# Optimization experiments

Measured on AMD Instinct MI355X. Metric: run time of the kernel, lower is better.

Reference implementation:

```python
import jax, jax.numpy as jnp
import numpy as np

EPS = 1e-5
RATIO = 8


def _conv3d(x, w, b, groups=1, pad=0):
    # x: [N,C,T,H,W], w: [O, C//groups, kT,kH,kW]
    y = jax.lax.conv_general_dilated(
        x, w, window_strides=(1, 1, 1), padding=[(pad, pad)] * 3,
        dimension_numbers=("NCDHW", "OIDHW", "NCDHW"), feature_group_count=groups)
    return y + b[None, :, None, None, None]


def _dwblock(x, pw1_w, pw1_b, dw_w, dw_b, pw2_w, pw2_b):
    # pointwise1 (1x1x1) -> depthwise 3x3x3 -> pointwise2 (1x1x1)
    mid = pw1_w.shape[0]
    x = _conv3d(x, pw1_w, pw1_b)
    x = _conv3d(x, dw_w, dw_b, groups=mid, pad=1)
    x = _conv3d(x, pw2_w, pw2_b)
    return x


def _make_dw_params(key, c_in, c_out, prefix):
    mid = c_in // RATIO
    ks = jax.random.split(key, 3)
    s = 0.02
    return {
        f"{prefix}_pw1_w": jax.random.normal(ks[0], (mid, c_in, 1, 1, 1), jnp.float32) * s,
        f"{prefix}_pw1_b": jnp.zeros((mid,), jnp.float32),
        f"{prefix}_dw_w": jax.random.normal(ks[1], (mid, 1, 3, 3, 3), jnp.float32) * s,
        f"{prefix}_dw_b": jnp.zeros((mid,), jnp.float32),
        f"{prefix}_pw2_w": jax.random.normal(ks[2], (c_out, mid, 1, 1, 1), jnp.float32) * s,
        f"{prefix}_pw2_b": jnp.zeros((c_out,), jnp.float32),
    }


def setup_inputs() -> dict:
    key = jax.random.key(0)
    N, C, T, H, W = 4, 256, 16, 28, 28
    KC, VC = 128, 256
    k0, k1, k2, k3, k4 = jax.random.split(key, 5)
    inp = {"input_": jax.random.normal(k0, (N, C, T, H, W), jnp.float32)}
    inp.update(_make_dw_params(k1, C, KC, "k"))
    inp.update(_make_dw_params(k2, C, KC, "q"))
    inp.update(_make_dw_params(k3, C, VC, "v"))
    inp.update(_make_dw_params(k4, VC, C, "r"))
    return inp


HEAD_COUNT = 8


def reference(input_,
              k_pw1_w, k_pw1_b, k_dw_w, k_dw_b, k_pw2_w, k_pw2_b,
              q_pw1_w, q_pw1_b, q_dw_w, q_dw_b, q_pw2_w, q_pw2_b,
              v_pw1_w, v_pw1_b, v_dw_w, v_dw_b, v_pw2_w, v_pw2_b,
              r_pw1_w, r_pw1_b, r_dw_w, r_dw_b, r_pw2_w, r_pw2_b):
    n, c, t, h, w = input_.shape
    L = t * h * w
    Hc = HEAD_COUNT

    keys = _dwblock(input_, k_pw1_w, k_pw1_b, k_dw_w, k_dw_b, k_pw2_w, k_pw2_b)
    queries = _dwblock(input_, q_pw1_w, q_pw1_b, q_dw_w, q_dw_b, q_pw2_w, q_pw2_b)
    values = _dwblock(input_, v_pw1_w, v_pw1_b, v_dw_w, v_dw_b, v_pw2_w, v_pw2_b)

    kc = keys.shape[1]
    vc = values.shape[1]
    hk, hv = kc // Hc, vc // Hc

    # [n, heads, head_dim, L]
    K = keys.reshape(n, Hc, hk, L)
    Q = queries.reshape(n, Hc, hk, L)
    V = values.reshape(n, Hc, hv, L)

    K = jax.nn.softmax(K, axis=3)          # softmax over sequence (dim=2 in torch slice)
    Q = jax.nn.softmax(Q, axis=2)          # softmax over per-head key channels (dim=1)

    # context = K @ V^T : [n, heads, hk, hv]
    context = jnp.einsum("nhkl,nhvl->nhkv", K, V)
    # attended = context^T @ Q : [n, heads, hv, L]
    attended = jnp.einsum("nhkv,nhkl->nhvl", context, Q)
    aggregated = attended.reshape(n, vc, t, h, w)

    reproj = _dwblock(aggregated, r_pw1_w, r_pw1_b, r_dw_w, r_dw_b, r_pw2_w, r_pw2_b)
    x = reproj + input_
    # f.layer_norm(x, x.size()): normalize over the WHOLE tensor, no affine
    mu = jnp.mean(x)
    var = jnp.mean((x - mu) ** 2)
    return (x - mu) / jnp.sqrt(var + EPS)
```

## Files before the change

### kernel.cpp

```cpp
#include <hip/hip_runtime.h>
#include <cstddef>

#define NB   4
#define CIN  256
#define TT   16
#define HH   28
#define WW   28
#define LL   12544
#define MIDC 32
#define KCC  128
#define VCC  256
#define HC   8
#define HK   16
#define HV   32
#define CTXSPLIT 14
#define CTXSTR 544
#define EPSV 1e-5f
#define XPAD 264

typedef __attribute__((ext_vector_type(8))) short bf16x8;
typedef __attribute__((ext_vector_type(8))) unsigned short u16x8;
typedef __attribute__((ext_vector_type(4))) float f32x4;
typedef __attribute__((ext_vector_type(4))) unsigned short u16x4;

__device__ __forceinline__ float b2f(unsigned short u) {
    return __builtin_bit_cast(float, ((unsigned int)u) << 16);
}
__device__ __forceinline__ unsigned short f2b(float f) {
    unsigned int u = __builtin_bit_cast(unsigned int, f);
    u += 0x7FFFu + ((u >> 16) & 1u);
    return (unsigned short)(u >> 16);
}

#define XTF_N_STRIDE 3211264ull
#define MID_SET_STRIDE 1605632ull

struct WconvA { const float* w1[4]; const float* w2[4]; };
struct Pw1M  { const short* wt[3]; const float* b[3]; unsigned short* out[3]; };
struct DwA   { const unsigned short* in[3]; const float* w[3]; const float* b[3]; unsigned short* out[3]; };
struct Pw2M  { const short* w2f; const unsigned short* d; const float* b[3]; unsigned short* out[3]; };

__global__ __launch_bounds__(256) void wconv_kernel(WconvA a, short* __restrict__ w1f,
                                                    short* __restrict__ w2f)
{
    const int g = blockIdx.x*256 + threadIdx.x;
    if (g < 4096) {
        const int L = g & 63, kap = (g >> 6) & 7, mt = (g >> 9) & 1, set = g >> 10;
        const int m = 16*mt + (L & 15);
        const int c0 = 32*kap + 8*(L >> 4);
        const float* wp = a.w1[set] + m*CIN + c0;
#pragma unroll
        for (int j = 0; j < 8; ++j) w1f[(size_t)g*8 + j] = (short)f2b(wp[j]);
    } else if (g < 4096 + 3072) {
        const int g2 = g - 4096;
        const int L = g2 & 63, mtg = g2 >> 6;
        int set, mtl;
        if (mtg < 8)       { set = 0; mtl = mtg; }
        else if (mtg < 16) { set = 1; mtl = mtg - 8; }
        else if (mtg < 32) { set = 2; mtl = mtg - 16; }
        else               { set = 3; mtl = mtg - 32; }
        const int m = 16*mtl + (L & 15);
        const int c0 = 8*(L >> 4);
        const float* wp = a.w2[set] + m*MIDC + c0;
#pragma unroll
        for (int j = 0; j < 8; ++j) w2f[(size_t)g2*8 + j] = (short)f2b(wp[j]);
    }
}

__global__ __launch_bounds__(128) void pw1_lds(const float* __restrict__ in, Pw1M a)
{
    __shared__ unsigned short xs[64*XPAD];
    const int n = blockIdx.y;
    const int l0 = blockIdx.x*64;
    const int t = threadIdx.x, wid = t >> 6, lane = t & 63;
    const float* ib = in + (size_t)n*CIN*LL;

    const int lt = (t & 15)*4;
    const int cp = (t >> 4)*2;
#pragma unroll 4
    for (int cc = 0; cc < 16; ++cc) {
        const int c = cc*16 + cp;
        float4 va = *reinterpret_cast<const float4*>(ib + (size_t)c*LL + l0 + lt);
        float4 vb = *reinterpret_cast<const float4*>(ib + (size_t)(c+1)*LL + l0 + lt);
        unsigned int p0 = (unsigned int)f2b(va.x) | ((unsigned int)f2b(vb.x) << 16);
        unsigned int p1 = (unsigned int)f2b(va.y) | ((unsigned int)f2b(vb.y) << 16);
        unsigned int p2 = (unsigned int)f2b(va.z) | ((unsigned int)f2b(vb.z) << 16);
        unsigned int p3 = (unsigned int)f2b(va.w) | ((unsigned int)f2b(vb.w) << 16);
        *reinterpret_cast<unsigned int*>(&xs[(lt+0)*XPAD + c]) = p0;
        *reinterpret_cast<unsigned int*>(&xs[(lt+1)*XPAD + c]) = p1;
        *reinterpret_cast<unsigned int*>(&xs[(lt+2)*XPAD + c]) = p2;
        *reinterpret_cast<unsigned int*>(&xs[(lt+3)*XPAD + c]) = p3;
    }
    __syncthreads();

    const int colb = lane & 15, qq = lane >> 4;
    f32x4 acc[3][2][2];
#pragma unroll
    for (int s = 0; s < 3; ++s)
#pragma unroll
        for (int mt = 0; mt < 2; ++mt)
#pragma unroll
            for (int ti = 0; ti < 2; ++ti)
#pragma unroll
                for (int r = 0; r < 4; ++r) acc[s][mt][ti][r] = 0.f;

    for (int kap = 0; kap < 8; ++kap) {
        bf16x8 bfr[2];
#pragma unroll
        for (int ti = 0; ti < 2; ++ti) {
            const int ll = (wid*2 + ti)*16 + colb;
            bfr[ti] = *reinterpret_cast<const bf16x8*>(&xs[ll*XPAD + kap*32 + 8*qq]);
        }
#pragma unroll
        for (int s = 0; s < 3; ++s) {
#pragma unroll
            for (int mt = 0; mt < 2; ++mt) {
                bf16x8 afr = *reinterpret_cast<const bf16x8*>(
                    a.wt[s] + ((mt*8 + kap)*512 + lane*8));
#pragma unroll
                for (int ti = 0; ti < 2; ++ti)
                    acc[s][mt][ti] = __builtin_amdgcn_mfma_f32_16x16x32_bf16(
                        afr, bfr[ti], acc[s][mt][ti], 0, 0, 0);
            }
        }
    }
#pragma unroll
    for (int s = 0; s < 3; ++s) {
        const float* bb = a.b[s];
        unsigned short* op = a.out[s] + (size_t)n*MIDC*LL;
#pragma unroll
        for (int mt = 0; mt < 2; ++mt) {
            const int m0 = mt*16 + qq*4;
#pragma unroll
            for (int ti = 0; ti < 2; ++ti) {
                const int lg = l0 + (wid*2 + ti)*16 + colb;
#pragma unroll
                for (int r = 0; r < 4; ++r)
                    op[(size_t)(m0 + r)*LL + lg] = f2b(acc[s][mt][ti][r] + bb[m0 + r]);
            }
        }
    }
}

__global__ __launch_bounds__(256) void pw1_frag(const short* __restrict__ xtf, Pw1M a)
{
    const int n = blockIdx.y, bx = blockIdx.x;
    const int t = threadIdx.x, wid = t >> 6, lane = t & 63;
    const int mt = wid & 1, lh = wid >> 1;
    const int tau0 = bx*8 + lh*4;
    const short* xb = xtf + (size_t)n*XTF_N_STRIDE;

    f32x4 acc[4];
#pragma unroll
    for (int i = 0; i < 4; ++i)
#pragma unroll
        for (int r = 0; r < 4; ++r) acc[i][r] = 0.f;

    for (int kap = 0; kap < 8; ++kap) {
        bf16x8 afr = *reinterpret_cast<const bf16x8*>(a.wt[0] + ((mt*8 + kap)*512 + lane*8));
#pragma unroll
        for (int i = 0; i < 4; ++i) {
            bf16x8 bfr = *reinterpret_cast<const bf16x8*>(
                xb + ((size_t)((tau0 + i)*8 + kap)*512 + lane*8));
            acc[i] = __builtin_amdgcn_mfma_f32_16x16x32_bf16(afr, bfr, acc[i], 0, 0, 0);
        }
    }
    const float* bb = a.b[0];
    unsigned short* op = a.out[0] + (size_t)n*MIDC*LL;
    const int col = lane & 15;
    const int m0 = mt*16 + (lane >> 4)*4;
#pragma unroll
    for (int r = 0; r < 4; ++r) {
        const float bv = bb[m0 + r];
#pragma unroll
        for (int i = 0; i < 4; ++i)
            op[(size_t)(m0 + r)*LL + (tau0 + i)*16 + col] = f2b(acc[i][r] + bv);
    }
}

struct Row6 { float v[6]; };

__device__ __forceinline__ Row6 load_row(const unsigned short* base, int zz, int yy, int x0)
{
    Row6 r;
    const bool ok = (zz >= 0) && (zz < TT) && (yy >= 0) && (yy < HH);
    if (ok) {
        const unsigned short* p = base + zz*(HH*WW) + yy*WW + x0;
        u16x4 m4 = *reinterpret_cast<const u16x4*>(p);
        r.v[0] = (x0 > 0)  ? b2f(p[-1]) : 0.f;
        r.v[1] = b2f(m4[0]); r.v[2] = b2f(m4[1]);
        r.v[3] = b2f(m4[2]); r.v[4] = b2f(m4[3]);
        r.v[5] = (x0 < 24) ? b2f(p[4]) : 0.f;
    } else {
#pragma unroll
        for (int i = 0; i < 6; ++i) r.v[i] = 0.f;
    }
    return r;
}

__device__ __forceinline__ void acc9(float& a0, float& a1, float& a2, float& a3,
                                     const Row6* rows, const float* w9)
{
#pragma unroll
    for (int dy = 0; dy < 3; ++dy)
#pragma unroll
        for (int dx = 0; dx < 3; ++dx) {
            const float wv = w9[dy*3 + dx];
            a0 = fmaf(wv, rows[dy].v[0 + dx], a0);
            a1 = fmaf(wv, rows[dy].v[1 + dx], a1);
            a2 = fmaf(wv, rows[dy].v[2 + dx], a2);
            a3 = fmaf(wv, rows[dy].v[3 + dx], a3);
        }
}

__global__ __launch_bounds__(256) void dw_reg(DwA a)
{
    const int tid = threadIdx.x;
    if (tid >= 196) return;
    const int z  = blockIdx.z;
    const int nm = blockIdx.y;
    const int m  = nm & (MIDC-1);
    const int t0 = blockIdx.x * 8;

    const float* wp = a.w[z] + m*27;
    float wv[27];
#pragma unroll
    for (int i = 0; i < 27; ++i) wv[i] = wp[i];
    const float bias = a.b[z][m];

    const int xg = tid % 7, y = tid / 7;
    const int x0 = xg*4;
    const unsigned short* ip = a.in[z] + (size_t)nm*LL;
    unsigned short* op = a.out[z] + (size_t)nm*LL;

    Row6 win[3][3];
#pragma unroll
    for (int dy = 0; dy < 3; ++dy) {
        win[0][dy] = load_row(ip, t0-1, y+dy-1, x0);
        win[1][dy] = load_row(ip, t0,   y+dy-1, x0);
    }
#pragma unroll
    for (int tt = 0; tt < 8; ++tt) {
        const int p0 = tt % 3, p1 = (tt+1) % 3, p2 = (tt+2) % 3;
        const int znew = t0 + tt + 1;
        win[p2][0] = load_row(ip, znew, y-1, x0);
        win[p2][1] = load_row(ip, znew, y,   x0);
        win[p2][2] = load_row(ip, znew, y+1, x0);

        float a0 = bias, a1 = bias, a2 = bias, a3 = bias;
        acc9(a0, a1, a2, a3, win[p0], wv);
        acc9(a0, a1, a2, a3, win[p1], wv + 9);
        acc9(a0, a1, a2, a3, win[p2], wv + 18);

        u16x4 o4 = { f2b(a0), f2b(a1), f2b(a2), f2b(a3) };
        *reinterpret_cast<u16x4*>(op + (size_t)(t0+tt)*(HH*WW) + y*WW + x0) = o4;
    }
}

__global__ __launch_bounds__(256) void pw2_g(Pw2M a)
{
    const int z = blockIdx.z, n = blockIdx.y, bx = blockIdx.x;
    int set, chunk;
    if (z < 2)      { set = 0; chunk = z; }
    else if (z < 4) { set = 1; chunk = z - 2; }
    else            { set = 2; chunk = z - 4; }
    const int OC   = (set == 2) ? 256 : 128;
    const int off2 = (set == 0) ? 0 : (set == 1) ? 8 : 16;

    const int t = threadIdx.x, wid = t >> 6, lane = t & 63;
    const int mtile = chunk*4 + wid;
    bf16x8 afr = *reinterpret_cast<const bf16x8*>(
        a.w2f + ((size_t)(off2 + mtile)*512 + lane*8));
    const unsigned short* db = a.d + (size_t)set*MID_SET_STRIDE + (size_t)n*MIDC*LL;
    const int colb = lane & 15, c0 = 8*(lane >> 4);

    f32x4 acc[4];
#pragma unroll
    for (int i = 0; i < 4; ++i) {
#pragma unroll
        for (int r = 0; r < 4; ++r) acc[i][r] = 0.f;
        const unsigned short* p = db + (size_t)c0*LL + (bx*4 + i)*16 + colb;
        bf16x8 bfr;
#pragma unroll
        for (int j = 0; j < 8; ++j) bfr[j] = (short)p[(size_t)j*LL];
        acc[i] = __builtin_amdgcn_mfma_f32_16x16x32_bf16(afr, bfr, acc[i], 0, 0, 0);
    }
    const float* bb = a.b[set];
    unsigned short* op = a.out[set] + (size_t)n*OC*LL;
    const int m0 = 16*mtile + (lane >> 4)*4;
#pragma unroll
    for (int r = 0; r < 4; ++r) {
        const float bv = bb[m0 + r];
#pragma unroll
        for (int i = 0; i < 4; ++i)
            op[(size_t)(m0 + r)*LL + (bx*4 + i)*16 + colb] = f2b(acc[i][r] + bv);
    }
}

__global__ __launch_bounds__(256) void ctx_mfma(
    const unsigned short* __restrict__ Kb, const unsigned short* __restrict__ Vb,
    float* __restrict__ ctxp)
{
    const int nh = blockIdx.y;
    const int sp = blockIdx.x;
    const int n = nh >> 3, h = nh & 7;
    const int t = threadIdx.x, w = t >> 6, lane = t & 63;
    const int i = lane & 15, q = lane >> 4;

    const unsigned short* Kp = Kb + ((size_t)(n*KCC + h*HK))*LL;
    const unsigned short* Vp = Vb + ((size_t)(n*VCC + h*HV))*LL;

    f32x4 a0 = {0.f,0.f,0.f,0.f}, a1 = {0.f,0.f,0.f,0.f};
    float asum = 0.f;

    const int cbase = sp*28 + w*7;
#pragma unroll 2
    for (int cc = 0; cc < 7; ++cc) {
        const int l0 = (cbase + cc)*32 + 8*q;
        bf16x8 kf = *reinterpret_cast<const bf16x8*>(Kp + (size_t)i*LL + l0);
        bf16x8 pf;
#pragma unroll
        for (int j = 0; j < 8; ++j) {
            const float e = __expf(b2f((unsigned short)kf[j]));
            asum += e;
            pf[j] = (short)f2b(e);
        }
        bf16x8 b0 = *reinterpret_cast<const bf16x8*>(Vp + (size_t)i*LL + l0);
        bf16x8 b1 = *reinterpret_cast<const bf16x8*>(Vp + (size_t)(i+16)*LL + l0);
        a0 = __builtin_amdgcn_mfma_f32_16x16x32_bf16(pf, b0, a0, 0, 0, 0);
        a1 = __builtin_amdgcn_mfma_f32_16x16x32_bf16(pf, b1, a1, 0, 0, 0);
    }
    asum += __shfl_xor(asum, 16);
    asum += __shfl_xor(asum, 32);

    __shared__ float cs[4][512];
    __shared__ float as[4][16];
#pragma unroll
    for (int r = 0; r < 4; ++r) {
        cs[w][(q*4 + r)*32 + i]      = a0[r];
        cs[w][(q*4 + r)*32 + 16 + i] = a1[r];
    }
    if (q == 0) as[w][i] = asum;
    __syncthreads();
    float* cp = ctxp + ((size_t)nh*CTXSPLIT + sp)*CTXSTR;
    for (int p = t; p < 512; p += 256)
        cp[p] = cs[0][p] + cs[1][p] + cs[2][p] + cs[3][p];
    if (t < 16) cp[512 + t] = as[0][t] + as[1][t] + as[2][t] + as[3][t];
}

__global__ void ctx_reduce(const float* __restrict__ ctxp, float* __restrict__ ctx)
{
    const int idx = blockIdx.x*256 + threadIdx.x;
    const int nh = idx >> 9;
    const int p  = idx & 511;
    const int k  = p >> 5;
    float s = 0.f, se = 0.f;
    for (int sp = 0; sp < CTXSPLIT; ++sp) {
        const float* cp = ctxp + ((size_t)nh*CTXSPLIT + sp)*CTXSTR;
        s  += cp[p];
        se += cp[512 + k];
    }
    ctx[idx] = s / se;
}

__global__ __launch_bounds__(256) void attended_kernel(
    const float* __restrict__ ctx, const unsigned short* __restrict__ Qb,
    short* __restrict__ aggf)
{
    const int nh = blockIdx.y;
    const int n = nh >> 3, h = nh & 7;
    const int l = blockIdx.x*256 + threadIdx.x;
    const float* __restrict__ cl = ctx + (size_t)nh*512;

    const unsigned short* Qp = Qb + ((size_t)(n*KCC + h*HK))*LL + l;
    float q[HK];
    float mx = -1e30f;
#pragma unroll
    for (int k = 0; k < HK; ++k) { q[k] = b2f(Qp[(size_t)k*LL]); mx = fmaxf(mx, q[k]); }
    float s = 0.f;
#pragma unroll
    for (int k = 0; k < HK; ++k) { q[k] = __expf(q[k] - mx); s += q[k]; }
    const float inv = 1.f / s;
#pragma unroll
    for (int k = 0; k < HK; ++k) q[k] *= inv;

    float av[HV];
#pragma unroll 4
    for (int v = 0; v < HV; ++v) {
        float acc = 0.f;
#pragma unroll
        for (int k = 0; k < HK; ++k) acc += q[k] * cl[k*HV + v];
        av[v] = acc;
    }
    short* ob = aggf + (size_t)n*XTF_N_STRIDE + ((size_t)((l >> 4)*8 + h))*512;
#pragma unroll
    for (int qd = 0; qd < 4; ++qd) {
        bf16x8 vv;
#pragma unroll
        for (int j = 0; j < 8; ++j) vv[j] = (short)f2b(av[qd*8 + j]);
        *reinterpret_cast<bf16x8*>(ob + (qd*16 + (l & 15))*8) = vv;
    }
}

__global__ __launch_bounds__(256) void pw2r_g(
    const unsigned short* __restrict__ d, const short* __restrict__ w2f,
    const float* __restrict__ bias, const float* __restrict__ resid,
    unsigned short* __restrict__ xout, float* __restrict__ part)
{
    const int z = blockIdx.z, n = blockIdx.y, bx = blockIdx.x;
    const int t = threadIdx.x, wid = t >> 6, lane = t & 63;
    const int mtile = z*4 + wid;
    bf16x8 afr = *reinterpret_cast<const bf16x8*>(
        w2f + ((size_t)(32 + mtile)*512 + lane*8));
    const unsigned short* db = d + (size_t)n*MIDC*LL;
    const int colb = lane & 15, c0 = 8*(lane >> 4);

    f32x4 acc[4];
#pragma unroll
    for (int i = 0; i < 4; ++i) {
#pragma unroll
        for (int r = 0; r < 4; ++r) acc[i][r] = 0.f;
        const unsigned short* p = db + (size_t)c0*LL + (bx*4 + i)*16 + colb;
        bf16x8 bfr;
#pragma unroll
        for (int j = 0; j < 8; ++j) bfr[j] = (short)p[(size_t)j*LL];
        acc[i] = __builtin_amdgcn_mfma_f32_16x16x32_bf16(afr, bfr, acc[i], 0, 0, 0);
    }
    const int m0 = 16*mtile + (lane >> 4)*4;
    float s1 = 0.f, s2 = 0.f;
#pragma unroll
    for (int r = 0; r < 4; ++r) {
        const float bv = bias[m0 + r];
#pragma unroll
        for (int i = 0; i < 4; ++i) {
            const size_t off = (size_t)(n*CIN + m0 + r)*LL + (bx*4 + i)*16 + colb;
            const float v = acc[i][r] + bv + resid[off];
            xout[off] = f2b(v);
            s1 += v; s2 += v*v;
        }
    }
    __shared__ float red[256];
    const int bid = (z*NB + n)*196 + bx;
    red[t] = s1; __syncthreads();
    for (int s = 128; s > 0; s >>= 1) { if (t < s) red[t] += red[t+s]; __syncthreads(); }
    if (t == 0) part[2*bid] = red[0];
    __syncthreads();
    red[t] = s2; __syncthreads();
    for (int s = 128; s > 0; s >>= 1) { if (t < s) red[t] += red[t+s]; __syncthreads(); }
    if (t == 0) part[2*bid + 1] = red[0];
}

__global__ void stats_kernel(const float* __restrict__ part, int nblocks,
                             float* __restrict__ stats)
{
    __shared__ float r1[256], r2[256];
    const int t = threadIdx.x;
    float s1 = 0.f, s2 = 0.f;
    for (int i = t; i < nblocks; i += 256) { s1 += part[2*i]; s2 += part[2*i+1]; }
    r1[t] = s1; r2[t] = s2; __syncthreads();
    for (int s = 128; s > 0; s >>= 1) { if (t < s) { r1[t] += r1[t+s]; r2[t] += r2[t+s]; } __syncthreads(); }
    if (t == 0) {
        const float M = (float)NB*CIN*LL;
        const float mu = r1[0]/M;
        const float var = r2[0]/M - mu*mu;
        stats[0] = mu;
        stats[1] = 1.0f/sqrtf(var + EPSV);
    }
}

__global__ __launch_bounds__(256) void norm_bf16(
    const unsigned short* __restrict__ x, const float* __restrict__ stats,
    float* __restrict__ out)
{
    const float mu = stats[0], inv = stats[1];
    const size_t total = (size_t)NB*CIN*LL;
    for (size_t i = ((size_t)blockIdx.x*256 + threadIdx.x)*8; i < total;
         i += (size_t)gridDim.x*256*8) {
        u16x8 v = *reinterpret_cast<const u16x8*>(x + i);
        float4 o0, o1;
        o0.x = (b2f(v[0])-mu)*inv; o0.y = (b2f(v[1])-mu)*inv;
        o0.z = (b2f(v[2])-mu)*inv; o0.w = (b2f(v[3])-mu)*inv;
        o1.x = (b2f(v[4])-mu)*inv; o1.y = (b2f(v[5])-mu)*inv;
        o1.z = (b2f(v[6])-mu)*inv; o1.w = (b2f(v[7])-mu)*inv;
        *reinterpret_cast<float4*>(out + i)     = o0;
        *reinterpret_cast<float4*>(out + i + 4) = o1;
    }
}

extern "C" void kernel_launch(void* const* d_in, const int* in_sizes, int n_in,
                              void* d_out, int out_size, void* d_ws, size_t ws_size,
                              hipStream_t stream) {
    const float* input   = (const float*)d_in[0];
    const float* k_pw1_w = (const float*)d_in[1];
    const float* k_pw1_b = (const float*)d_in[2];
    const float* k_dw_w  = (const float*)d_in[3];
    const float* k_dw_b  = (const float*)d_in[4];
    const float* k_pw2_w = (const float*)d_in[5];
    const float* k_pw2_b = (const float*)d_in[6];
    const float* q_pw1_w = (const float*)d_in[7];
    const float* q_pw1_b = (const float*)d_in[8];
    const float* q_dw_w  = (const float*)d_in[9];
    const float* q_dw_b  = (const float*)d_in[10];
    const float* q_pw2_w = (const float*)d_in[11];
    const float* q_pw2_b = (const float*)d_in[12];
    const float* v_pw1_w = (const float*)d_in[13];
    const float* v_pw1_b = (const float*)d_in[14];
    const float* v_dw_w  = (const float*)d_in[15];
    const float* v_dw_b  = (const float*)d_in[16];
    const float* v_pw2_w = (const float*)d_in[17];
    const float* v_pw2_b = (const float*)d_in[18];
    const float* r_pw1_w = (const float*)d_in[19];
    const float* r_pw1_b = (const float*)d_in[20];
    const float* r_dw_w  = (const float*)d_in[21];
    const float* r_dw_b  = (const float*)d_in[22];
    const float* r_pw2_w = (const float*)d_in[23];
    const float* r_pw2_b = (const float*)d_in[24];

    char* base = (char*)d_ws;
    unsigned short* dbuf = (unsigned short*)base;
    short* aggf = (short*)base;
    unsigned short* midb  = (unsigned short*)(base + 25690112);
    unsigned short* mid_r = midb;
    unsigned short* d_r   = (unsigned short*)(base + 25690112 + 6422528);
    unsigned short* Kb = (unsigned short*)(base + 54591488);
    unsigned short* Qb = (unsigned short*)(base + 67436544);
    unsigned short* Vb = (unsigned short*)(base + 80281600);
    unsigned short* xb = (unsigned short*)(base + 54591488);
    char* H = base + 105971712;
    float* ctxp   = (float*)H;
    float* ctx    = (float*)(H + 974848);
    float* part   = (float*)(H + 1040384);
    float* statsp = (float*)(H + 1065472);
    short* w1f    = (short*)(H + 1065536);
    short* w2f    = (short*)(H + 1131072);

    {
        WconvA a;
        a.w1[0]=k_pw1_w; a.w1[1]=q_pw1_w; a.w1[2]=v_pw1_w; a.w1[3]=r_pw1_w;
        a.w2[0]=k_pw2_w; a.w2[1]=q_pw2_w; a.w2[2]=v_pw2_w; a.w2[3]=r_pw2_w;
        wconv_kernel<<<28, 256, 0, stream>>>(a, w1f, w2f);
    }
    {
        Pw1M a;
        a.wt[0]=w1f;        a.wt[1]=w1f+8192;   a.wt[2]=w1f+16384;
        a.b[0]=k_pw1_b;     a.b[1]=q_pw1_b;     a.b[2]=v_pw1_b;
        a.out[0]=midb;      a.out[1]=midb+MID_SET_STRIDE; a.out[2]=midb+2*MID_SET_STRIDE;
        pw1_lds<<<dim3(196, NB), 128, 0, stream>>>(input, a);
    }
    {
        DwA a;
        a.in[0]=midb; a.in[1]=midb+MID_SET_STRIDE; a.in[2]=midb+2*MID_SET_STRIDE;
        a.w[0]=k_dw_w; a.w[1]=q_dw_w; a.w[2]=v_dw_w;
        a.b[0]=k_dw_b; a.b[1]=q_dw_b; a.b[2]=v_dw_b;
        a.out[0]=dbuf; a.out[1]=dbuf+MID_SET_STRIDE; a.out[2]=dbuf+2*MID_SET_STRIDE;
        dw_reg<<<dim3(2, NB*MIDC, 3), 256, 0, stream>>>(a);
    }
    {
        Pw2M a;
        a.w2f = w2f; a.d = dbuf;
        a.b[0]=k_pw2_b; a.b[1]=q_pw2_b; a.b[2]=v_pw2_b;
        a.out[0]=Kb; a.out[1]=Qb; a.out[2]=Vb;
        pw2_g<<<dim3(196, NB, 8), 256, 0, stream>>>(a);
    }
    ctx_mfma<<<dim3(CTXSPLIT, NB*HC), 256, 0, stream>>>(Kb, Vb, ctxp);
    ctx_reduce<<<64, 256, 0, stream>>>(ctxp, ctx);
    attended_kernel<<<dim3(49, NB*HC), 256, 0, stream>>>(ctx, Qb, aggf);
    {
        Pw1M a;
        a.wt[0]=w1f+24576; a.wt[1]=a.wt[0]; a.wt[2]=a.wt[0];
        a.b[0]=r_pw1_b;    a.b[1]=a.b[0];   a.b[2]=a.b[0];
        a.out[0]=mid_r;    a.out[1]=a.out[0]; a.out[2]=a.out[0];
        pw1_frag<<<dim3(98, NB), 256, 0, stream>>>(aggf, a);
    }
    {
        DwA a;
        a.in[0]=mid_r; a.w[0]=r_dw_w; a.b[0]=r_dw_b; a.out[0]=d_r;
        a.in[1]=a.in[0]; a.w[1]=a.w[0]; a.b[1]=a.b[0]; a.out[1]=a.out[0];
        a.in[2]=a.in[0]; a.w[2]=a.w[0]; a.b[2]=a.b[0]; a.out[2]=a.out[0];
        dw_reg<<<dim3(2, NB*MIDC, 1), 256, 0, stream>>>(a);
    }
    pw2r_g<<<dim3(196, NB, 4), 256, 0, stream>>>(d_r, w2f, r_pw2_b, input, xb, part);
    stats_kernel<<<1, 256, 0, stream>>>(part, 3136, statsp);
    norm_bf16<<<2048, 256, 0, stream>>>(xb, statsp, (float*)d_out);
}
```

Baseline: 143.5 us.

## Fuse attention apply with reproj pw1 and replace reduce kernels with atomics

The context partial sums are now accumulated with atomicAdd into a buffer zeroed inside wconv_kernel, which removes ctx_reduce. The attended computation is fused with the reprojection pointwise1 MFMA through an LDS tile, so the bf16 aggregated tensor no longer round-trips through global memory. The global layer-norm statistics are reduced by atomics into 8 slots that norm_bf16 reads directly, which removes stats_kernel. Together this cuts three launches and one large intermediate buffer. The cost is that float atomics make the sums order-nondeterministic, and the large LDS tile may lower occupancy of the fused kernel.

```diff
diff --git a/kernel.cpp b/kernel.cpp
--- a/kernel.cpp
+++ b/kernel.cpp
@@ -14,9 +14,9 @@
 #define HK   16
 #define HV   32
 #define CTXSPLIT 14
-#define CTXSTR 544
 #define EPSV 1e-5f
 #define XPAD 264
+#define APAD 264
 
 typedef __attribute__((ext_vector_type(8))) short bf16x8;
 typedef __attribute__((ext_vector_type(8))) unsigned short u16x8;
@@ -32,7 +32,6 @@
     return (unsigned short)(u >> 16);
 }
 
-#define XTF_N_STRIDE 3211264ull
 #define MID_SET_STRIDE 1605632ull
 
 struct WconvA { const float* w1[4]; const float* w2[4]; };
@@ -41,9 +40,11 @@
 struct Pw2M  { const short* w2f; const unsigned short* d; const float* b[3]; unsigned short* out[3]; };
 
 __global__ __launch_bounds__(256) void wconv_kernel(WconvA a, short* __restrict__ w1f,
-                                                    short* __restrict__ w2f)
+                                                    short* __restrict__ w2f,
+                                                    float* __restrict__ zbuf)
 {
     const int g = blockIdx.x*256 + threadIdx.x;
+    for (int i = g; i < 16912; i += 28*256) zbuf[i] = 0.f;
     if (g < 4096) {
         const int L = g & 63, kap = (g >> 6) & 7, mt = (g >> 9) & 1, set = g >> 10;
         const int m = 16*mt + (L & 15);
@@ -142,42 +143,6 @@
     }
 }
 
-__global__ __launch_bounds__(256) void pw1_frag(const short* __restrict__ xtf, Pw1M a)
-{
-    const int n = blockIdx.y, bx = blockIdx.x;
-    const int t = threadIdx.x, wid = t >> 6, lane = t & 63;
-    const int mt = wid & 1, lh = wid >> 1;
-    const int tau0 = bx*8 + lh*4;
-    const short* xb = xtf + (size_t)n*XTF_N_STRIDE;
-
-    f32x4 acc[4];
-#pragma unroll
-    for (int i = 0; i < 4; ++i)
-#pragma unroll
-        for (int r = 0; r < 4; ++r) acc[i][r] = 0.f;
-
-    for (int kap = 0; kap < 8; ++kap) {
-        bf16x8 afr = *reinterpret_cast<const bf16x8*>(a.wt[0] + ((mt*8 + kap)*512 + lane*8));
-#pragma unroll
-        for (int i = 0; i < 4; ++i) {
-            bf16x8 bfr = *reinterpret_cast<const bf16x8*>(
-                xb + ((size_t)((tau0 + i)*8 + kap)*512 + lane*8));
-            acc[i] = __builtin_amdgcn_mfma_f32_16x16x32_bf16(afr, bfr, acc[i], 0, 0, 0);
-        }
-    }
-    const float* bb = a.b[0];
-    unsigned short* op = a.out[0] + (size_t)n*MIDC*LL;
-    const int col = lane & 15;
-    const int m0 = mt*16 + (lane >> 4)*4;
-#pragma unroll
-    for (int r = 0; r < 4; ++r) {
-        const float bv = bb[m0 + r];
-#pragma unroll
-        for (int i = 0; i < 4; ++i)
-            op[(size_t)(m0 + r)*LL + (tau0 + i)*16 + col] = f2b(acc[i][r] + bv);
-    }
-}
-
 struct Row6 { float v[6]; };
 
 __device__ __forceinline__ Row6 load_row(const unsigned short* base, int zz, int yy, int x0)
@@ -299,7 +264,7 @@
 
 __global__ __launch_bounds__(256) void ctx_mfma(
     const unsigned short* __restrict__ Kb, const unsigned short* __restrict__ Vb,
-    float* __restrict__ ctxp)
+    float* __restrict__ csum, float* __restrict__ sesum)
 {
     const int nh = blockIdx.y;
     const int sp = blockIdx.x;
@@ -342,70 +307,107 @@
     }
     if (q == 0) as[w][i] = asum;
     __syncthreads();
-    float* cp = ctxp + ((size_t)nh*CTXSPLIT + sp)*CTXSTR;
+    float* cp = csum + (size_t)nh*512;
     for (int p = t; p < 512; p += 256)
-        cp[p] = cs[0][p] + cs[1][p] + cs[2][p] + cs[3][p];
-    if (t < 16) cp[512 + t] = as[0][t] + as[1][t] + as[2][t] + as[3][t];
-}
-
-__global__ void ctx_reduce(const float* __restrict__ ctxp, float* __restrict__ ctx)
-{
-    const int idx = blockIdx.x*256 + threadIdx.x;
-    const int nh = idx >> 9;
-    const int p  = idx & 511;
-    const int k  = p >> 5;
-    float s = 0.f, se = 0.f;
-    for (int sp = 0; sp < CTXSPLIT; ++sp) {
-        const float* cp = ctxp + ((size_t)nh*CTXSPLIT + sp)*CTXSTR;
-        s  += cp[p];
-        se += cp[512 + k];
-    }
-    ctx[idx] = s / se;
-}
-
-__global__ __launch_bounds__(256) void attended_kernel(
-    const float* __restrict__ ctx, const unsigned short* __restrict__ Qb,
-    short* __restrict__ aggf)
-{
-    const int nh = blockIdx.y;
-    const int n = nh >> 3, h = nh & 7;
-    const int l = blockIdx.x*256 + threadIdx.x;
-    const float* __restrict__ cl = ctx + (size_t)nh*512;
-
-    const unsigned short* Qp = Qb + ((size_t)(n*KCC + h*HK))*LL + l;
-    float q[HK];
-    float mx = -1e30f;
-#pragma unroll
-    for (int k = 0; k < HK; ++k) { q[k] = b2f(Qp[(size_t)k*LL]); mx = fmaxf(mx, q[k]); }
-    float s = 0.f;
-#pragma unroll
-    for (int k = 0; k < HK; ++k) { q[k] = __expf(q[k] - mx); s += q[k]; }
-    const float inv = 1.f / s;
-#pragma unroll
-    for (int k = 0; k < HK; ++k) q[k] *= inv;
-
-    float av[HV];
+        atomicAdd(&cp[p], cs[0][p] + cs[1][p] + cs[2][p] + cs[3][p]);
+    if (t < 16)
+        atomicAdd(&sesum[nh*16 + t], as[0][t] + as[1][t] + as[2][t] + as[3][t]);
+}
+
+__global__ __launch_bounds__(256) void att_pw1r(
+    const unsigned short* __restrict__ Qb,
+    const float* __restrict__ csum, const float* __restrict__ sesum,
+    const short* __restrict__ w1fr, const float* __restrict__ b1r,
+    unsigned short* __restrict__ mid_r)
+{
+    __shared__ short aggt[128*APAD];
+    const int n = blockIdx.y, bx = blockIdx.x;
+    const int t = threadIdx.x;
+    const int l0 = bx*128;
+
+    for (int ph = 0; ph < 4; ++ph) {
+        const int id = ph*256 + t;
+        const int l = id & 127, h = id >> 7;
+        const int nh = n*HC + h;
+        const unsigned short* Qp = Qb + ((size_t)(n*KCC + h*HK))*LL + l0 + l;
+        float q[HK];
+        float mx = -1e30f;
+#pragma unroll
+        for (int k = 0; k < HK; ++k) { q[k] = b2f(Qp[(size_t)k*LL]); mx = fmaxf(mx, q[k]); }
+        float s = 0.f;
+#pragma unroll
+        for (int k = 0; k < HK; ++k) { q[k] = __expf(q[k] - mx); s += q[k]; }
+        const float inv = 1.f / s;
+        const float* __restrict__ cl = csum + (size_t)nh*512;
+        const float* __restrict__ sl = sesum + nh*16;
+        float qf[HK];
+#pragma unroll
+        for (int k = 0; k < HK; ++k) qf[k] = q[k]*inv / sl[k];
+
+        float av[HV];
 #pragma unroll 4
-    for (int v = 0; v < HV; ++v) {
-        float acc = 0.f;
-#pragma unroll
-        for (int k = 0; k < HK; ++k) acc += q[k] * cl[k*HV + v];
-        av[v] = acc;
-    }
-    short* ob = aggf + (size_t)n*XTF_N_STRIDE + ((size_t)((l >> 4)*8 + h))*512;
-#pragma unroll
-    for (int qd = 0; qd < 4; ++qd) {
-        bf16x8 vv;
-#pragma unroll
-        for (int j = 0; j < 8; ++j) vv[j] = (short)f2b(av[qd*8 + j]);
-        *reinterpret_cast<bf16x8*>(ob + (qd*16 + (l & 15))*8) = vv;
+        for (int v = 0; v < HV; ++v) {
+            float acc = 0.f;
+#pragma unroll
+            for (int k = 0; k < HK; ++k) acc += qf[k] * cl[k*HV + v];
+            av[v] = acc;
+        }
+        short* row = &aggt[l*APAD + h*32];
+#pragma unroll
+        for (int qd = 0; qd < 4; ++qd) {
+            bf16x8 vv;
+#pragma unroll
+            for (int j = 0; j < 8; ++j) vv[j] = (short)f2b(av[qd*8 + j]);
+            *reinterpret_cast<bf16x8*>(row + qd*8) = vv;
+        }
+    }
+    __syncthreads();
+
+    const int wid = t >> 6, lane = t & 63;
+    const int colb = lane & 15, qq = lane >> 4;
+    f32x4 acc[2][2];
+#pragma unroll
+    for (int mt = 0; mt < 2; ++mt)
+#pragma unroll
+        for (int ti = 0; ti < 2; ++ti)
+#pragma unroll
+            for (int r = 0; r < 4; ++r) acc[mt][ti][r] = 0.f;
+
+    for (int kap = 0; kap < 8; ++kap) {
+        bf16x8 bfr[2];
+#pragma unroll
+        for (int ti = 0; ti < 2; ++ti) {
+            const int ll = (wid*2 + ti)*16 + colb;
+            bfr[ti] = *reinterpret_cast<const bf16x8*>(&aggt[ll*APAD + kap*32 + 8*qq]);
+        }
+#pragma unroll
+        for (int mt = 0; mt < 2; ++mt) {
+            bf16x8 afr = *reinterpret_cast<const bf16x8*>(
+                w1fr + ((mt*8 + kap)*512 + lane*8));
+#pragma unroll
+            for (int ti = 0; ti < 2; ++ti)
+                acc[mt][ti] = __builtin_amdgcn_mfma_f32_16x16x32_bf16(
+                    afr, bfr[ti], acc[mt][ti], 0, 0, 0);
+        }
+    }
+    unsigned short* op = mid_r + (size_t)n*MIDC*LL;
+#pragma unroll
+    for (int mt = 0; mt < 2; ++mt) {
+        const int m0 = mt*16 + qq*4;
+#pragma unroll
+        for (int ti = 0; ti < 2; ++ti) {
+            const int lg = l0 + (wid*2 + ti)*16 + colb;
+#pragma unroll
+            for (int r = 0; r < 4; ++r)
+                op[(size_t)(m0 + r)*LL + lg] = f2b(acc[mt][ti][r] + b1r[m0 + r]);
+        }
     }
 }
 
 __global__ __launch_bounds__(256) void pw2r_g(
     const unsigned short* __restrict__ d, const short* __restrict__ w2f,
     const float* __restrict__ bias, const float* __restrict__ resid,
-    unsigned short* __restrict__ xout, float* __restrict__ part)
+    unsigned short* __restrict__ xout, float* __restrict__ statacc)
 {
     const int z = blockIdx.z, n = blockIdx.y, bx = blockIdx.x;
     const int t = threadIdx.x, wid = t >> 6, lane = t & 63;
@@ -440,39 +442,29 @@
         }
     }
     __shared__ float red[256];
-    const int bid = (z*NB + n)*196 + bx;
     red[t] = s1; __syncthreads();
     for (int s = 128; s > 0; s >>= 1) { if (t < s) red[t] += red[t+s]; __syncthreads(); }
-    if (t == 0) part[2*bid] = red[0];
+    float blk1 = red[0];
     __syncthreads();
     red[t] = s2; __syncthreads();
     for (int s = 128; s > 0; s >>= 1) { if (t < s) red[t] += red[t+s]; __syncthreads(); }
-    if (t == 0) part[2*bid + 1] = red[0];
-}
-
-__global__ void stats_kernel(const float* __restrict__ part, int nblocks,
-                             float* __restrict__ stats)
-{
-    __shared__ float r1[256], r2[256];
-    const int t = threadIdx.x;
-    float s1 = 0.f, s2 = 0.f;
-    for (int i = t; i < nblocks; i += 256) { s1 += part[2*i]; s2 += part[2*i+1]; }
-    r1[t] = s1; r2[t] = s2; __syncthreads();
-    for (int s = 128; s > 0; s >>= 1) { if (t < s) { r1[t] += r1[t+s]; r2[t] += r2[t+s]; } __syncthreads(); }
     if (t == 0) {
-        const float M = (float)NB*CIN*LL;
-        const float mu = r1[0]/M;
-        const float var = r2[0]/M - mu*mu;
-        stats[0] = mu;
-        stats[1] = 1.0f/sqrtf(var + EPSV);
+        const int slot = ((z*NB + n)*196 + bx) & 7;
+        atomicAdd(&statacc[2*slot],     blk1);
+        atomicAdd(&statacc[2*slot + 1], red[0]);
     }
 }
 
 __global__ __launch_bounds__(256) void norm_bf16(
-    const unsigned short* __restrict__ x, const float* __restrict__ stats,
+    const unsigned short* __restrict__ x, const float* __restrict__ statacc,
     float* __restrict__ out)
 {
-    const float mu = stats[0], inv = stats[1];
+    float S1 = 0.f, S2 = 0.f;
+#pragma unroll
+    for (int i = 0; i < 8; ++i) { S1 += statacc[2*i]; S2 += statacc[2*i+1]; }
+    const float M = (float)NB*CIN*LL;
+    const float mu = S1/M;
+    const float inv = rsqrtf(S2/M - mu*mu + EPSV);
     const size_t total = (size_t)NB*CIN*LL;
     for (size_t i = ((size_t)blockIdx.x*256 + threadIdx.x)*8; i < total;
          i += (size_t)gridDim.x*256*8) {
@@ -518,7 +510,6 @@
 
     char* base = (char*)d_ws;
     unsigned short* dbuf = (unsigned short*)base;
-    short* aggf = (short*)base;
     unsigned short* midb  = (unsigned short*)(base + 25690112);
     unsigned short* mid_r = midb;
     unsigned short* d_r   = (unsigned short*)(base + 25690112 + 6422528);
@@ -527,18 +518,17 @@
     unsigned short* Vb = (unsigned short*)(base + 80281600);
     unsigned short* xb = (unsigned short*)(base + 54591488);
     char* H = base + 105971712;
-    float* ctxp   = (float*)H;
-    float* ctx    = (float*)(H + 974848);
-    float* part   = (float*)(H + 1040384);
-    float* statsp = (float*)(H + 1065472);
-    short* w1f    = (short*)(H + 1065536);
-    short* w2f    = (short*)(H + 1131072);
+    float* csum    = (float*)H;
+    float* sesum   = (float*)(H + 65536);
+    float* statacc = (float*)(H + 67584);
+    short* w1f     = (short*)(H + 67712);
+    short* w2f     = (short*)(H + 133248);
 
     {
         WconvA a;
         a.w1[0]=k_pw1_w; a.w1[1]=q_pw1_w; a.w1[2]=v_pw1_w; a.w1[3]=r_pw1_w;
         a.w2[0]=k_pw2_w; a.w2[1]=q_pw2_w; a.w2[2]=v_pw2_w; a.w2[3]=r_pw2_w;
-        wconv_kernel<<<28, 256, 0, stream>>>(a, w1f, w2f);
+        wconv_kernel<<<28, 256, 0, stream>>>(a, w1f, w2f, csum);
     }
     {
         Pw1M a;
@@ -562,16 +552,9 @@
         a.out[0]=Kb; a.out[1]=Qb; a.out[2]=Vb;
         pw2_g<<<dim3(196, NB, 8), 256, 0, stream>>>(a);
     }
-    ctx_mfma<<<dim3(CTXSPLIT, NB*HC), 256, 0, stream>>>(Kb, Vb, ctxp);
-    ctx_reduce<<<64, 256, 0, stream>>>(ctxp, ctx);
-    attended_kernel<<<dim3(49, NB*HC), 256, 0, stream>>>(ctx, Qb, aggf);
-    {
-        Pw1M a;
-        a.wt[0]=w1f+24576; a.wt[1]=a.wt[0]; a.wt[2]=a.wt[0];
-        a.b[0]=r_pw1_b;    a.b[1]=a.b[0];   a.b[2]=a.b[0];
-        a.out[0]=mid_r;    a.out[1]=a.out[0]; a.out[2]=a.out[0];
-        pw1_frag<<<dim3(98, NB), 256, 0, stream>>>(aggf, a);
-    }
+    ctx_mfma<<<dim3(CTXSPLIT, NB*HC), 256, 0, stream>>>(Kb, Vb, csum, sesum);
+    att_pw1r<<<dim3(98, NB), 256, 0, stream>>>(Qb, csum, sesum,
+                                               w1f + 24576, r_pw1_b, mid_r);
     {
         DwA a;
         a.in[0]=mid_r; a.w[0]=r_dw_w; a.b[0]=r_dw_b; a.out[0]=d_r;
@@ -579,7 +562,6 @@
         a.in[2]=a.in[0]; a.w[2]=a.w[0]; a.b[2]=a.b[0]; a.out[2]=a.out[0];
         dw_reg<<<dim3(2, NB*MIDC, 1), 256, 0, stream>>>(a);
     }
-    pw2r_g<<<dim3(196, NB, 4), 256, 0, stream>>>(d_r, w2f, r_pw2_b, input, xb, part);
-    stats_kernel<<<1, 256, 0, stream>>>(part, 3136, statsp);
-    norm_bf16<<<2048, 256, 0, stream>>>(xb, statsp, (float*)d_out);
-}
+    pw2r_g<<<dim3(196, NB, 4), 256, 0, stream>>>(d_r, w2f, r_pw2_b, input, xb, statacc);
+    norm_bf16<<<2048, 256, 0, stream>>>(xb, statacc, (float*)d_out);
+}
```

New measurement: 216.5 us. 1.51x slower.
